# Performance work log

Measured on AMD Instinct MI355X. Metric: run time of the kernel, lower is better.

The kernel has to match this reference:

```python
import jax, jax.numpy as jnp
import numpy as np

V, DS, DF, H, NPASS = 32000, 64, 256, 8, 2
B, L, NB = 2, 1024, 512
EPS = 1e-5


def setup_inputs() -> dict:
    ks = jax.random.split(jax.random.key(0), 20)
    def n(k, shape, scale=0.02):
        return (scale * jax.random.normal(k, shape)).astype(jnp.float32)
    return {
        "token_ids": jax.random.randint(ks[0], (B, L), 0, V),
        "tok_mu": n(ks[1], (V, DS)),
        "tok_log_var": n(ks[2], (V, DS)),
        "tok_raw_alpha": n(ks[3], (V, 1), 1.0),
        "tok_features": n(ks[4], (V, DF)),
        "pos_mu": n(ks[5], (L, DS)),
        "qproj_w": n(ks[6], (H * DS, DS)),
        "qproj_b": jnp.zeros((H * DS,), jnp.float32),
        "hproj_w": n(ks[7], (DF, H * DF)),
        "hproj_b": jnp.zeros((DF,), jnp.float32),
        "mu_up_w": n(ks[8], (DS, 2 * DF)),
        "mu_up_b": jnp.zeros((DS,), jnp.float32),
        "agate_w": n(ks[9], (1, 2 * DF)),
        "agate_b": jnp.zeros((1,), jnp.float32),
        "ffn_w": n(ks[10], (DF, 2 * DF)),
        "ffn_b": jnp.zeros((DF,), jnp.float32),
        "ln_g": jnp.ones((DF,), jnp.float32),
        "ln_b": jnp.zeros((DF,), jnp.float32),
        "lm_w": n(ks[11], (V, DF)),
        "lm_b": jnp.zeros((V,), jnp.float32),
        "blob_mu": n(ks[12], (NB, DS)),
        "blob_lv": n(ks[13], (NB, DS)),
        "blob_ra": n(ks[14], (NB,), 1.0),
        "blob_f": n(ks[15], (NB, DF)),
        "bgate_w": n(ks[16], (1, 2 * DF)),
        "bgate_b": jnp.zeros((1,), jnp.float32),
    }


def _composite_weights(a):
    # front-to-back alpha compositing along last axis: w_j = a_j * prod_{k<j}(1-a_k)
    T = jnp.cumprod(1.0 - a, axis=-1)
    T_ex = jnp.concatenate([jnp.ones_like(T[..., :1]), T[..., :-1]], axis=-1)
    return a * T_ex, T[..., -1]


def _forward(token_ids, tok_mu, tok_log_var, tok_raw_alpha, tok_features, pos_mu,
             qproj_w, qproj_b, hproj_w, hproj_b, mu_up_w, mu_up_b, agate_w, agate_b,
             ffn_w, ffn_b, ln_g, ln_b, lm_w, lm_b, blob_mu, blob_lv, blob_ra, blob_f,
             bgate_w, bgate_b):
    Bc, Lc = token_ids.shape
    mu = tok_mu[token_ids] + pos_mu[:Lc][None]          # [B,L,DS]
    log_var = tok_log_var[token_ids]                     # [B,L,DS]
    alpha = jax.nn.sigmoid(tok_raw_alpha[token_ids][..., 0])  # [B,L]
    features = tok_features[token_ids]                   # [B,L,DF]

    # ---- blob query + blob render ----
    query = mu.mean(axis=1)                              # [B,DS]
    iv_b = jnp.exp(-blob_lv)                             # [NB,DS]
    d2b = (jnp.einsum('bd,nd->bn', query * query, iv_b)
           - 2.0 * jnp.einsum('bd,nd->bn', query, blob_mu * iv_b)
           + jnp.sum(blob_mu * blob_mu * iv_b, -1)[None])
    Kb = jnp.exp(-0.5 * d2b)                             # [B,NB]
    ab = jax.nn.sigmoid(blob_ra)[None] * Kb              # effective alpha
    wb, t_residual = _composite_weights(ab)
    blob_meaning = jnp.einsum('bn,nf->bf', wb, blob_f)   # [B,DF] (blob_proj = Identity)

    # ---- word meaning: multi-pass Gaussian causal render ----
    mask = jnp.tril(jnp.ones((Lc, Lc), jnp.float32))
    iv = jnp.exp(-log_var)                               # inv-variance, fixed across passes
    cur_mu, cur_alpha, cur_feat = mu, alpha, features
    meaning = None
    for p in range(NPASS):
        q = (cur_mu @ qproj_w.T + qproj_b).reshape(Bc, Lc, H, DS).transpose(0, 2, 1, 3)  # [B,H,L,DS]
        # squared Mahalanobis distance via three GEMM-style contractions (no [B,H,L,L,DS] tensor)
        d2 = (jnp.einsum('bhid,bjd->bhij', q * q, iv)
              - 2.0 * jnp.einsum('bhid,bjd->bhij', q, cur_mu * iv)
              + jnp.sum(cur_mu * cur_mu * iv, -1)[:, None, None, :])
        K = jnp.exp(-0.5 * d2)                           # [B,H,L,L]
        a = cur_alpha[:, None, None, :] * K * mask
        w, _ = _composite_weights(a)
        m = jnp.einsum('bhij,bjf->bhif', w, cur_feat)    # [B,H,L,DF]
        m_cat = m.transpose(0, 2, 1, 3).reshape(Bc, Lc, H * DF)
        meaning = m_cat @ hproj_w.T + hproj_b            # [B,L,DF] (dropout = eval/identity)
        if p < NPASS - 1:
            ctx = jnp.concatenate([cur_feat, meaning], axis=-1)  # [B,L,2DF]
            cur_mu = cur_mu + ctx @ mu_up_w.T + mu_up_b
            cur_alpha = cur_alpha * jax.nn.sigmoid(ctx @ agate_w.T + agate_b)[..., 0]
            cur_feat = cur_feat + ctx @ ffn_w.T + ffn_b

    # ---- blob gate fusion ----
    blob_exp = jnp.broadcast_to(blob_meaning[:, None, :], meaning.shape)
    gate = jax.nn.sigmoid(jnp.concatenate([blob_exp, meaning], -1) @ bgate_w.T + bgate_b)  # [B,L,1]
    t_res = t_residual[:, None, None]
    fused = (1.0 - t_res) * gate * blob_exp + t_res * meaning

    # ---- final layernorm + lm head ----
    mean = fused.mean(-1, keepdims=True)
    var = ((fused - mean) ** 2).mean(-1, keepdims=True)
    h = (fused - mean) * jax.lax.rsqrt(var + EPS) * ln_g + ln_b
    logits = h @ lm_w.T + lm_b                           # [B,L,V]
    return logits


def reference(token_ids, tok_mu, tok_log_var, tok_raw_alpha, tok_features, pos_mu,
              qproj_w, qproj_b, hproj_w, hproj_b, mu_up_w, mu_up_b, agate_w, agate_b,
              ffn_w, ffn_b, ln_g, ln_b, lm_w, lm_b, blob_mu, blob_lv, blob_ra, blob_f,
              bgate_w, bgate_b):
    return _forward(token_ids, tok_mu, tok_log_var, tok_raw_alpha, tok_features, pos_mu,
                    qproj_w, qproj_b, hproj_w, hproj_b, mu_up_w, mu_up_b, agate_w, agate_b,
                    ffn_w, ffn_b, ln_g, ln_b, lm_w, lm_b, blob_mu, blob_lv, blob_ra, blob_f,
                    bgate_w, bgate_b)
```

## Files before the change

kernel.cpp:

```cpp
#include <hip/hip_runtime.h>
#include <hip/hip_bf16.h>
#include <cstdint>
#include <cstddef>

#define V_   32000
#define DS_  64
#define DF_  256
#define H_   8
#define L_   1024
#define B_   2
#define NB_  512
#define BL_  2048
#define EPS_ 1e-5f

typedef unsigned short ushort_t;
typedef unsigned int uint_t;
typedef short bf16x8 __attribute__((ext_vector_type(8)));
typedef float f32x4 __attribute__((ext_vector_type(4)));
#define AS1 __attribute__((address_space(1)))
#define AS3 __attribute__((address_space(3)))

__device__ __forceinline__ float sigmoidf_(float x) { return 1.f / (1.f + __expf(-x)); }
__device__ __forceinline__ ushort_t f2bf(float x) {
    __hip_bfloat16 b = __float2bfloat16(x);
    return __builtin_bit_cast(ushort_t, b);
}
__device__ __forceinline__ uint_t packbf(float lo, float hi) {
    return ((uint_t)f2bf(hi) << 16) | (uint_t)f2bf(lo);
}
__device__ __forceinline__ float bflo(uint_t v) {
    return __builtin_bit_cast(float, v << 16);
}
__device__ __forceinline__ float bfhi(uint_t v) {
    return __builtin_bit_cast(float, v & 0xFFFF0000u);
}

__device__ __forceinline__ float block_reduce_sum(float v, float* red) {
    int t = threadIdx.x;
    red[t] = v;
    __syncthreads();
    for (int s = 128; s > 0; s >>= 1) {
        if (t < s) red[t] += red[t + s];
        __syncthreads();
    }
    float r = red[0];
    __syncthreads();
    return r;
}

__global__ __launch_bounds__(256) void k_cvt5(
    const float* __restrict__ s0, ushort_t* __restrict__ d0,
    const float* __restrict__ s1, ushort_t* __restrict__ d1,
    const float* __restrict__ s2, ushort_t* __restrict__ d2,
    const float* __restrict__ s3, ushort_t* __restrict__ d3,
    const float* __restrict__ s4, ushort_t* __restrict__ d4) {
    int blk = blockIdx.x;
    const float* s; ushort_t* d; int base;
    if (blk < 32)        { s = s0; d = d0; base = blk; }
    else if (blk < 64)   { s = s1; d = d1; base = blk - 32; }
    else if (blk < 192)  { s = s2; d = d2; base = blk - 64; }
    else if (blk < 704)  { s = s3; d = d3; base = blk - 192; }
    else                 { s = s4; d = d4; base = blk - 704; }
    int i = (base * 256 + threadIdx.x) * 4;
    float4 v = *reinterpret_cast<const float4*>(s + i);
    ushort4 o = {f2bf(v.x), f2bf(v.y), f2bf(v.z), f2bf(v.w)};
    *reinterpret_cast<ushort4*>(d + i) = o;
}

__global__ __launch_bounds__(256) void k_gather(
    const int* __restrict__ tok, const float* __restrict__ tok_mu,
    const float* __restrict__ tok_lv, const float* __restrict__ tok_ra,
    const float* __restrict__ tok_f, const float* __restrict__ pos_mu,
    float* __restrict__ mu, ushort_t* __restrict__ mub16,
    uint_t* __restrict__ muivP, float* __restrict__ alpha,
    float* __restrict__ feat, ushort_t* __restrict__ featb16,
    uint_t* __restrict__ featP) {
    __shared__ float sfg[256];
    int row = blockIdx.x;
    int l = row & (L_ - 1);
    int t = threadIdx.x;
    int v = tok[row];
    if (t < DS_) {
        float m = tok_mu[(size_t)v * DS_ + t] + pos_mu[l * DS_ + t];
        mu[(size_t)row * DS_ + t] = m;
        mub16[(size_t)row * DS_ + t] = f2bf(m);
        float ivv = __expf(-tok_lv[(size_t)v * DS_ + t]);
        muivP[(size_t)t * BL_ + row] = packbf(m, ivv);
    }
    float fv = tok_f[(size_t)v * DF_ + t];
    feat[(size_t)row * DF_ + t] = fv;
    featb16[(size_t)row * DF_ + t] = f2bf(fv);
    sfg[t] = fv;
    if (t == 0) alpha[row] = sigmoidf_(tok_ra[v]);
    __syncthreads();
    if (t < 128) {
        int half = t >> 6, fl = t & 63;
        featP[(size_t)row * 128 + half * 64 + fl] =
            packbf(sfg[half * 128 + fl], sfg[half * 128 + fl + 64]);
    }
}

__global__ __launch_bounds__(256) void k_queryblob(
    const float* __restrict__ mu, const float* __restrict__ blob_mu,
    const float* __restrict__ blob_lv, const float* __restrict__ blob_ra,
    const float* __restrict__ blob_f, float* __restrict__ blobm,
    float* __restrict__ tres) {
    __shared__ float red[256];
    __shared__ float sq[DS_];
    __shared__ float sa[NB_];
    __shared__ float sp[NB_];
    int b = blockIdx.x, t = threadIdx.x;
    int d = t & 63, c = t >> 6;
    float s = 0.f;
    for (int l = c; l < L_; l += 4) s += mu[((size_t)b * L_ + l) * DS_ + d];
    red[t] = s;
    __syncthreads();
    if (c == 0)
        sq[d] = (red[d] + red[64 + d] + red[128 + d] + red[192 + d]) * (1.f / L_);
    __syncthreads();
    for (int n = t; n < NB_; n += 256) {
        float d2 = 0.f;
        for (int dd = 0; dd < DS_; ++dd) {
            float diff = sq[dd] - blob_mu[n * DS_ + dd];
            d2 += __expf(-blob_lv[n * DS_ + dd]) * diff * diff;
        }
        float a = sigmoidf_(blob_ra[n]) * __expf(-0.5f * d2);
        sa[n] = a;
        sp[n] = 1.f - a;
    }
    __syncthreads();
    int n0 = t, n1 = t + 256;
    for (int s2 = 1; s2 < NB_; s2 <<= 1) {
        float t0 = (n0 >= s2) ? sp[n0 - s2] : 1.f;
        float t1 = (n1 >= s2) ? sp[n1 - s2] : 1.f;
        __syncthreads();
        sp[n0] *= t0;
        sp[n1] *= t1;
        __syncthreads();
    }
    float w0 = sa[n0] * (n0 ? sp[n0 - 1] : 1.f);
    float w1 = sa[n1] * sp[n1 - 1];
    __syncthreads();
    sa[n0] = w0;
    sa[n1] = w1;
    if (t == 0) tres[b] = sp[NB_ - 1];
    __syncthreads();
    float acc = 0.f;
    for (int n = 0; n < NB_; ++n) acc += sa[n] * blob_f[n * DF_ + t];
    blobm[b * DF_ + t] = acc;
}

__global__ __launch_bounds__(512) void k_attn3(
    const float* __restrict__ q, const uint_t* __restrict__ muivP,
    const float* __restrict__ alpha, const uint_t* __restrict__ featP,
    ushort_t* __restrict__ mcatb) {
    __shared__ uint_t smiu[64 * 64];
    __shared__ uint_t sfp[64 * 128];
    __shared__ float sq[H_][64];
    __shared__ float swt[H_][64];
    __shared__ float sT[H_];
    int tid = threadIdx.x;
    int w = tid >> 6, lane = tid & 63;
    int bid = blockIdx.x;
    int b = bid >> 10, i = bid & (L_ - 1);
    int row = b * L_ + i;

    sq[w][lane] = q[(size_t)row * 512 + tid];
    float T = 1.f;
    float a0 = 0.f, a1 = 0.f, a2 = 0.f, a3 = 0.f;

    for (int j0 = 0; j0 <= i; j0 += 64) {
        __syncthreads();
        if (j0 > 0) {
            bool alive = false;
            #pragma unroll
            for (int h = 0; h < H_; ++h) alive |= (sT[h] >= 1e-12f);
            if (!alive) break;
        }
        {
            const uint_t* src = muivP + b * L_ + j0;
            #pragma unroll
            for (int r = 0; r < 2; ++r) {
                int d = w * 8 + r * 4 + (lane >> 4);
                const uint_t* gp = src + (size_t)d * BL_ + (lane & 15) * 4;
                __builtin_amdgcn_global_load_lds((const AS1 uint_t*)gp,
                    (AS3 uint_t*)&smiu[(w * 8 + r * 4) * 64], 16, 0, 0);
            }
            const uint_t* fsrc = featP + (size_t)(b * L_ + j0) * 128 + w * 1024;
            #pragma unroll
            for (int it = 0; it < 4; ++it) {
                __builtin_amdgcn_global_load_lds((const AS1 uint_t*)(fsrc + it * 256 + lane * 4),
                    (AS3 uint_t*)&sfp[w * 1024 + it * 256], 16, 0, 0);
            }
        }
        __syncthreads();

        int jj = j0 + lane;
        float d2 = 0.f;
        #pragma unroll 8
        for (int d = 0; d < 64; ++d) {
            uint_t v = smiu[d * 64 + lane];
            float m = bflo(v), iv = bfhi(v);
            float diff = sq[w][d] - m;
            d2 = fmaf(iv * diff, diff, d2);
        }
        float a = (jj <= i) ? alpha[b * L_ + jj] * __expf(-0.5f * d2) : 0.f;

        float p = 1.f - a;
        #pragma unroll
        for (int s = 1; s < 64; s <<= 1) {
            float tt = __shfl_up(p, s, 64);
            if (lane >= s) p *= tt;
        }
        float Tex = __shfl_up(p, 1, 64);
        if (lane == 0) Tex = 1.f;
        swt[w][lane] = a * T * Tex;
        float Tch = __shfl(p, 63, 64);
        unsigned long long dead = __ballot(p < 1e-12f);
        int jn = i - j0 + 1;
        if (jn > 64) jn = 64;
        if (dead) {
            int cut = __builtin_ctzll(dead) + 1;
            if (cut < jn) jn = cut;
        }
        T *= Tch;
        if (lane == 0) sT[w] = T;

        for (int j = 0; j < jn; ++j) {
            float wj = swt[w][j];
            uint_t v0 = sfp[j * 128 + lane];
            uint_t v1 = sfp[j * 128 + 64 + lane];
            a0 = fmaf(wj, bflo(v0), a0);
            a1 = fmaf(wj, bfhi(v0), a1);
            a2 = fmaf(wj, bflo(v1), a2);
            a3 = fmaf(wj, bfhi(v1), a3);
        }
    }
    ushort_t* o = mcatb + (size_t)row * 2048 + w * 256 + lane;
    o[0] = f2bf(a0); o[64] = f2bf(a1); o[128] = f2bf(a2); o[192] = f2bf(a3);
}

template <int BM, int BN, int BK, int WGM, int WGN, bool NTS, bool WB16>
__global__ __launch_bounds__(256) void gemm_mfma2(
    const ushort_t* __restrict__ A, const ushort_t* __restrict__ A2, int K1,
    int strideA, const ushort_t* __restrict__ W, const float* __restrict__ bias,
    float* __restrict__ C, ushort_t* __restrict__ Cb, int M, int N, int K) {
    constexpr int WMF = BM / WGM / 16;
    constexpr int WNF = BN / WGN / 16;
    constexpr int KK  = BK / 32;
    constexpr int AHALF = BM * BK;
    constexpr int BHALF = BN * BK;
    constexpr int STAGE_B = 2 * (AHALF + BHALF) * 2;
    constexpr int EPI_B = BM * BN * 4;
    constexpr int SMEM_B = STAGE_B > EPI_B ? STAGE_B : EPI_B;
    __shared__ __align__(16) char smem[SMEM_B];
    ushort_t* As = (ushort_t*)smem;
    ushort_t* Bs = (ushort_t*)(smem + 2 * AHALF * 2);

    const int tid = threadIdx.x;
    const int wave = tid >> 6, lane = tid & 63;
    const int m0 = blockIdx.x * BM, n0 = blockIdx.y * BN;
    const int wr = wave / WGN, wc = wave % WGN;
    const int lr = lane & 15;
    const int q4 = lane >> 4;

    f32x4 acc[WMF][WNF] = {};

    auto stage = [&](int buf, int t) {
        const int k0g = t * BK;
        const ushort_t* Abase = (A2 != nullptr && k0g >= K1) ? A2 : A;
        const int kof = (A2 != nullptr && k0g >= K1) ? k0g - K1 : k0g;
        ushort_t* Ad = As + buf * AHALF;
        #pragma unroll
        for (int it = 0; it < (BM * BK / 8) / 256; ++it) {
            int cbase = it * 256 + wave * 64;
            int c = cbase + lane;
            int r = c & (BM - 1), c8 = c / BM;
            const ushort_t* gp = Abase + (size_t)(m0 + r) * strideA + kof + c8 * 8;
            __builtin_amdgcn_global_load_lds((const AS1 uint_t*)gp,
                                             (AS3 uint_t*)(Ad + cbase * 8), 16, 0, 0);
        }
        ushort_t* Bd = Bs + buf * BHALF;
        #pragma unroll
        for (int it = 0; it < (BN * BK / 8) / 256; ++it) {
            int cbase = it * 256 + wave * 64;
            int c = cbase + lane;
            int r = c & (BN - 1), c8 = c / BN;
            const ushort_t* gp = W + (size_t)(n0 + r) * K + k0g + c8 * 8;
            __builtin_amdgcn_global_load_lds((const AS1 uint_t*)gp,
                                             (AS3 uint_t*)(Bd + cbase * 8), 16, 0, 0);
        }
    };

    const int nsteps = K / BK;
    stage(0, 0);
    __syncthreads();
    for (int t = 0; t < nsteps; ++t) {
        const int cur = t & 1;
        if (t + 1 < nsteps) stage(cur ^ 1, t + 1);
        const ushort_t* Ab = As + cur * AHALF;
        const ushort_t* Bb = Bs + cur * BHALF;
        bf16x8 af[WMF][KK], bfr[WNF][KK];
        #pragma unroll
        for (int mi = 0; mi < WMF; ++mi)
            #pragma unroll
            for (int kk = 0; kk < KK; ++kk)
                af[mi][kk] = *reinterpret_cast<const bf16x8*>(
                    &Ab[((kk * 4 + q4) * BM + wr * (BM / WGM) + mi * 16 + lr) * 8]);
        #pragma unroll
        for (int ni = 0; ni < WNF; ++ni)
            #pragma unroll
            for (int kk = 0; kk < KK; ++kk)
                bfr[ni][kk] = *reinterpret_cast<const bf16x8*>(
                    &Bb[((kk * 4 + q4) * BN + wc * (BN / WGN) + ni * 16 + lr) * 8]);
        #pragma unroll
        for (int kk = 0; kk < KK; ++kk)
            #pragma unroll
            for (int mi = 0; mi < WMF; ++mi)
                #pragma unroll
                for (int ni = 0; ni < WNF; ++ni)
                    acc[mi][ni] = __builtin_amdgcn_mfma_f32_16x16x32_bf16(
                        af[mi][kk], bfr[ni][kk], acc[mi][ni], 0, 0, 0);
        __syncthreads();
    }

    float* tile = (float*)smem;
    #pragma unroll
    for (int mi = 0; mi < WMF; ++mi)
        #pragma unroll
        for (int ni = 0; ni < WNF; ++ni) {
            int col = wc * (BN / WGN) + ni * 16 + lr;
            float bv = bias[n0 + col];
            #pragma unroll
            for (int j = 0; j < 4; ++j) {
                int r2 = wr * (BM / WGM) + mi * 16 + q4 * 4 + j;
                tile[r2 * BN + col] = acc[mi][ni][j] + bv;
            }
        }
    __syncthreads();
    constexpr int EV = (BM * BN / 4) / 256;
    #pragma unroll
    for (int e = 0; e < EV; ++e) {
        int idx = e * 256 + tid;
        int r = idx / (BN / 4), c4 = idx % (BN / 4);
        f32x4 v = reinterpret_cast<const f32x4*>(tile)[idx];
        f32x4* dst = reinterpret_cast<f32x4*>(&C[(size_t)(m0 + r) * N + n0 + c4 * 4]);
        if (NTS) __builtin_nontemporal_store(v, dst);
        else *dst = v;
        if (WB16) {
            ushort4 ob = {f2bf(v[0]), f2bf(v[1]), f2bf(v[2]), f2bf(v[3])};
            *reinterpret_cast<ushort4*>(&Cb[(size_t)(m0 + r) * N + n0 + c4 * 4]) = ob;
        }
    }
}

__global__ __launch_bounds__(256) void k_apply(
    const float* __restrict__ meaning, const float* __restrict__ agw,
    const float* __restrict__ agb, const float* __restrict__ dmu,
    const float* __restrict__ dffn, float* __restrict__ mu,
    ushort_t* __restrict__ mub16, uint_t* __restrict__ muivP,
    float* __restrict__ alpha, float* __restrict__ feat,
    ushort_t* __restrict__ featb16, uint_t* __restrict__ featP) {
    __shared__ float red[256];
    int row = blockIdx.x, t = threadIdx.x;
    float c0 = feat[(size_t)row * DF_ + t];
    float c1 = meaning[(size_t)row * DF_ + t];
    float s = block_reduce_sum(c0 * agw[t] + c1 * agw[256 + t], red);
    if (t == 0) alpha[row] *= sigmoidf_(s + agb[0]);
    if (t < DS_) {
        float m = mu[(size_t)row * DS_ + t] + dmu[(size_t)row * DS_ + t];
        mu[(size_t)row * DS_ + t] = m;
        mub16[(size_t)row * DS_ + t] = f2bf(m);
        uint_t v = muivP[(size_t)t * BL_ + row];
        muivP[(size_t)t * BL_ + row] = (v & 0xFFFF0000u) | (uint_t)f2bf(m);
    }
    float fn = c0 + dffn[(size_t)row * DF_ + t];
    feat[(size_t)row * DF_ + t] = fn;
    featb16[(size_t)row * DF_ + t] = f2bf(fn);
    red[t] = fn;
    __syncthreads();
    if (t < 128) {
        int half = t >> 6, fl = t & 63;
        featP[(size_t)row * 128 + half * 64 + fl] =
            packbf(red[half * 128 + fl], red[half * 128 + fl + 64]);
    }
}

__global__ __launch_bounds__(256) void k_fused_ln(
    const float* __restrict__ meaning, const float* __restrict__ blobm,
    const float* __restrict__ tres, const float* __restrict__ bgw,
    const float* __restrict__ bgb, const float* __restrict__ ln_g,
    const float* __restrict__ ln_b, ushort_t* __restrict__ houtb) {
    __shared__ float red[256];
    int row = blockIdx.x, t = threadIdx.x;
    int b = row >> 10;
    float m = meaning[(size_t)row * DF_ + t];
    float be = blobm[b * DF_ + t];
    float tr = tres[b];
    float gsum = block_reduce_sum(be * bgw[t] + m * bgw[256 + t], red);
    float gate = sigmoidf_(gsum + bgb[0]);
    float f = (1.f - tr) * gate * be + tr * m;
    float mean = block_reduce_sum(f, red) * (1.f / DF_);
    float d = f - mean;
    float var = block_reduce_sum(d * d, red) * (1.f / DF_);
    houtb[(size_t)row * DF_ + t] = f2bf(d * rsqrtf(var + EPS_) * ln_g[t] + ln_b[t]);
}

extern "C" void kernel_launch(void* const* d_in, const int* in_sizes, int n_in,
                              void* d_out, int out_size, void* d_ws, size_t ws_size,
                              hipStream_t stream) {
    const int*   tok      = (const int*)d_in[0];
    const float* tok_mu   = (const float*)d_in[1];
    const float* tok_lv   = (const float*)d_in[2];
    const float* tok_ra   = (const float*)d_in[3];
    const float* tok_f    = (const float*)d_in[4];
    const float* pos_mu   = (const float*)d_in[5];
    const float* qproj_w  = (const float*)d_in[6];
    const float* qproj_b  = (const float*)d_in[7];
    const float* hproj_w  = (const float*)d_in[8];
    const float* hproj_b  = (const float*)d_in[9];
    const float* mu_up_w  = (const float*)d_in[10];
    const float* mu_up_b  = (const float*)d_in[11];
    const float* agate_w  = (const float*)d_in[12];
    const float* agate_b  = (const float*)d_in[13];
    const float* ffn_w    = (const float*)d_in[14];
    const float* ffn_b    = (const float*)d_in[15];
    const float* ln_g     = (const float*)d_in[16];
    const float* ln_b     = (const float*)d_in[17];
    const float* lm_w     = (const float*)d_in[18];
    const float* lm_b     = (const float*)d_in[19];
    const float* blob_mu  = (const float*)d_in[20];
    const float* blob_lv  = (const float*)d_in[21];
    const float* blob_ra  = (const float*)d_in[22];
    const float* blob_f   = (const float*)d_in[23];
    const float* bgate_w  = (const float*)d_in[24];
    const float* bgate_b  = (const float*)d_in[25];
    float* out = (float*)d_out;

    float* ws = (float*)d_ws;
    float* mu      = ws;
    float* alpha   = mu + BL_ * DS_;
    float* feat    = alpha + BL_;
    float* blobm   = feat + BL_ * DF_;
    float* tres    = blobm + B_ * DF_;
    float* q       = tres + 64;
    float* meaning = q + BL_ * 512;
    float* dmu     = meaning + BL_ * DF_;
    float* dffn    = dmu + BL_ * DS_;
    uint_t* muivP  = (uint_t*)(dffn + BL_ * DF_);
    uint_t* featP  = muivP + (size_t)DS_ * BL_;
    ushort_t* mub16 = (ushort_t*)(featP + (size_t)BL_ * 128);
    ushort_t* featb16 = mub16 + (size_t)BL_ * DS_;
    ushort_t* meanb16 = featb16 + (size_t)BL_ * DF_;
    ushort_t* mcatb = meanb16 + (size_t)BL_ * DF_;
    ushort_t* hbufb = mcatb + (size_t)BL_ * 2048;
    ushort_t* wbf   = hbufb + (size_t)BL_ * DF_;
    ushort_t* hpwbf = wbf + (size_t)V_ * DF_;
    ushort_t* qpwbf = hpwbf + (size_t)DF_ * 2048;
    ushort_t* muwbf = qpwbf + (size_t)512 * 64;
    ushort_t* ffnwbf = muwbf + (size_t)64 * 512;

    k_cvt5<<<8704, 256, 0, stream>>>(qproj_w, qpwbf, mu_up_w, muwbf,
                                     ffn_w, ffnwbf, hproj_w, hpwbf, lm_w, wbf);

    k_gather<<<BL_, 256, 0, stream>>>(tok, tok_mu, tok_lv, tok_ra, tok_f, pos_mu,
                                      mu, mub16, muivP, alpha, feat, featb16, featP);
    k_queryblob<<<B_, 256, 0, stream>>>(mu, blob_mu, blob_lv, blob_ra, blob_f,
                                        blobm, tres);

    for (int p = 0; p < 2; ++p) {
        gemm_mfma2<32, 32, 64, 2, 2, false, false>
            <<<dim3(BL_ / 32, 512 / 32), 256, 0, stream>>>(
            mub16, nullptr, 0, DS_, qpwbf, qproj_b, q, nullptr, BL_, 512, DS_);
        k_attn3<<<BL_, 512, 0, stream>>>(q, muivP, alpha, featP, mcatb);
        if (p == 0) {
            gemm_mfma2<32, 32, 64, 2, 2, false, true>
                <<<dim3(BL_ / 32, DF_ / 32), 256, 0, stream>>>(
                mcatb, nullptr, 0, H_ * DF_, hpwbf, hproj_b, meaning, meanb16,
                BL_, DF_, H_ * DF_);
            gemm_mfma2<32, 32, 64, 2, 2, false, false>
                <<<dim3(BL_ / 32, DS_ / 32), 256, 0, stream>>>(
                featb16, meanb16, DF_, DF_, muwbf, mu_up_b, dmu, nullptr,
                BL_, DS_, 512);
            gemm_mfma2<32, 32, 64, 2, 2, false, false>
                <<<dim3(BL_ / 32, DF_ / 32), 256, 0, stream>>>(
                featb16, meanb16, DF_, DF_, ffnwbf, ffn_b, dffn, nullptr,
                BL_, DF_, 512);
            k_apply<<<BL_, 256, 0, stream>>>(meaning, agate_w, agate_b, dmu, dffn,
                                             mu, mub16, muivP, alpha, feat,
                                             featb16, featP);
        } else {
            gemm_mfma2<32, 32, 64, 2, 2, false, false>
                <<<dim3(BL_ / 32, DF_ / 32), 256, 0, stream>>>(
                mcatb, nullptr, 0, H_ * DF_, hpwbf, hproj_b, meaning, nullptr,
                BL_, DF_, H_ * DF_);
        }
    }

    k_fused_ln<<<BL_, 256, 0, stream>>>(meaning, blobm, tres, bgate_w, bgate_b,
                                        ln_g, ln_b, hbufb);
    gemm_mfma2<128, 128, 64, 2, 2, true, false>
        <<<dim3(BL_ / 128, V_ / 128), 256, 0, stream>>>(
        hbufb, nullptr, 0, DF_, wbf, lm_b, out, nullptr, BL_, V_, DF_);
}
```

Before: 332.4 us.

## Fuse setup kernels, compute query projection inside attention, merge mu/ffn GEMMs

Merges the weight conversion, token gather and blob-query kernels into one k_setup launch. The query-projection GEMM is dropped and q is computed in fp32 inside the attention kernel from mu and qproj_w. The mu_up and ffn GEMMs become a single 320-wide GEMM with concatenated weights and bias. The packed mu/ivar and feature layouts change to 8-byte pairs for wider LDS reads. This cuts launch count and intermediate traffic, at the cost of redundant per-block q computation and a mixed-role setup kernel where 256 of 512 threads sit idle in most blocks.

After: 376.9 us. 13.4% more time.

```diff
diff --git a/kernel.cpp b/kernel.cpp
--- a/kernel.cpp
+++ b/kernel.cpp
@@ -17,6 +17,7 @@
 typedef unsigned int uint_t;
 typedef short bf16x8 __attribute__((ext_vector_type(8)));
 typedef float f32x4 __attribute__((ext_vector_type(4)));
+typedef unsigned int uint2x __attribute__((ext_vector_type(2)));
 #define AS1 __attribute__((address_space(1)))
 #define AS3 __attribute__((address_space(3)))
 
@@ -48,114 +49,128 @@
     return r;
 }
 
-__global__ __launch_bounds__(256) void k_cvt5(
-    const float* __restrict__ s0, ushort_t* __restrict__ d0,
-    const float* __restrict__ s1, ushort_t* __restrict__ d1,
-    const float* __restrict__ s2, ushort_t* __restrict__ d2,
-    const float* __restrict__ s3, ushort_t* __restrict__ d3,
-    const float* __restrict__ s4, ushort_t* __restrict__ d4) {
-    int blk = blockIdx.x;
-    const float* s; ushort_t* d; int base;
-    if (blk < 32)        { s = s0; d = d0; base = blk; }
-    else if (blk < 64)   { s = s1; d = d1; base = blk - 32; }
-    else if (blk < 192)  { s = s2; d = d2; base = blk - 64; }
-    else if (blk < 704)  { s = s3; d = d3; base = blk - 192; }
-    else                 { s = s4; d = d4; base = blk - 704; }
-    int i = (base * 256 + threadIdx.x) * 4;
-    float4 v = *reinterpret_cast<const float4*>(s + i);
-    ushort4 o = {f2bf(v.x), f2bf(v.y), f2bf(v.z), f2bf(v.w)};
-    *reinterpret_cast<ushort4*>(d + i) = o;
-}
-
-__global__ __launch_bounds__(256) void k_gather(
+#define NCVT_   8672
+#define NGATH_  (NCVT_ + BL_)
+#define NQB_    (NGATH_ + B_)
+__global__ __launch_bounds__(512) void k_setup(
     const int* __restrict__ tok, const float* __restrict__ tok_mu,
     const float* __restrict__ tok_lv, const float* __restrict__ tok_ra,
     const float* __restrict__ tok_f, const float* __restrict__ pos_mu,
-    float* __restrict__ mu, ushort_t* __restrict__ mub16,
-    uint_t* __restrict__ muivP, float* __restrict__ alpha,
-    float* __restrict__ feat, ushort_t* __restrict__ featb16,
-    uint_t* __restrict__ featP) {
-    __shared__ float sfg[256];
-    int row = blockIdx.x;
-    int l = row & (L_ - 1);
-    int t = threadIdx.x;
-    int v = tok[row];
-    if (t < DS_) {
-        float m = tok_mu[(size_t)v * DS_ + t] + pos_mu[l * DS_ + t];
-        mu[(size_t)row * DS_ + t] = m;
-        mub16[(size_t)row * DS_ + t] = f2bf(m);
-        float ivv = __expf(-tok_lv[(size_t)v * DS_ + t]);
-        muivP[(size_t)t * BL_ + row] = packbf(m, ivv);
-    }
-    float fv = tok_f[(size_t)v * DF_ + t];
-    feat[(size_t)row * DF_ + t] = fv;
-    featb16[(size_t)row * DF_ + t] = f2bf(fv);
-    sfg[t] = fv;
-    if (t == 0) alpha[row] = sigmoidf_(tok_ra[v]);
-    __syncthreads();
-    if (t < 128) {
-        int half = t >> 6, fl = t & 63;
-        featP[(size_t)row * 128 + half * 64 + fl] =
-            packbf(sfg[half * 128 + fl], sfg[half * 128 + fl + 64]);
-    }
-}
-
-__global__ __launch_bounds__(256) void k_queryblob(
-    const float* __restrict__ mu, const float* __restrict__ blob_mu,
-    const float* __restrict__ blob_lv, const float* __restrict__ blob_ra,
-    const float* __restrict__ blob_f, float* __restrict__ blobm,
-    float* __restrict__ tres) {
-    __shared__ float red[256];
-    __shared__ float sq[DS_];
-    __shared__ float sa[NB_];
-    __shared__ float sp[NB_];
-    int b = blockIdx.x, t = threadIdx.x;
-    int d = t & 63, c = t >> 6;
-    float s = 0.f;
-    for (int l = c; l < L_; l += 4) s += mu[((size_t)b * L_ + l) * DS_ + d];
-    red[t] = s;
-    __syncthreads();
-    if (c == 0)
-        sq[d] = (red[d] + red[64 + d] + red[128 + d] + red[192 + d]) * (1.f / L_);
-    __syncthreads();
-    for (int n = t; n < NB_; n += 256) {
-        float d2 = 0.f;
-        for (int dd = 0; dd < DS_; ++dd) {
-            float diff = sq[dd] - blob_mu[n * DS_ + dd];
-            d2 += __expf(-blob_lv[n * DS_ + dd]) * diff * diff;
-        }
-        float a = sigmoidf_(blob_ra[n]) * __expf(-0.5f * d2);
-        sa[n] = a;
-        sp[n] = 1.f - a;
-    }
-    __syncthreads();
-    int n0 = t, n1 = t + 256;
-    for (int s2 = 1; s2 < NB_; s2 <<= 1) {
-        float t0 = (n0 >= s2) ? sp[n0 - s2] : 1.f;
-        float t1 = (n1 >= s2) ? sp[n1 - s2] : 1.f;
-        __syncthreads();
-        sp[n0] *= t0;
-        sp[n1] *= t1;
-        __syncthreads();
-    }
-    float w0 = sa[n0] * (n0 ? sp[n0 - 1] : 1.f);
-    float w1 = sa[n1] * sp[n1 - 1];
-    __syncthreads();
-    sa[n0] = w0;
-    sa[n1] = w1;
-    if (t == 0) tres[b] = sp[NB_ - 1];
-    __syncthreads();
-    float acc = 0.f;
-    for (int n = 0; n < NB_; ++n) acc += sa[n] * blob_f[n * DF_ + t];
-    blobm[b * DF_ + t] = acc;
-}
-
-__global__ __launch_bounds__(512) void k_attn3(
-    const float* __restrict__ q, const uint_t* __restrict__ muivP,
-    const float* __restrict__ alpha, const uint_t* __restrict__ featP,
+    const float* __restrict__ mu_up_w, const float* __restrict__ ffn_w,
+    const float* __restrict__ hproj_w, const float* __restrict__ lm_w,
+    const float* __restrict__ mu_up_b, const float* __restrict__ ffn_b,
+    const float* __restrict__ blob_mu, const float* __restrict__ blob_lv,
+    const float* __restrict__ blob_ra, const float* __restrict__ blob_f,
+    ushort_t* __restrict__ cwbf, ushort_t* __restrict__ hpwbf,
+    ushort_t* __restrict__ wbf, float* __restrict__ cbias,
+    float* __restrict__ mu, uint_t* __restrict__ muivP2,
+    float* __restrict__ alpha, float* __restrict__ feat,
+    ushort_t* __restrict__ featb16, uint2x* __restrict__ fArr,
+    float* __restrict__ blobm, float* __restrict__ tres) {
+    int blk = blockIdx.x;
+    int tid = threadIdx.x;
+    if (blk < NCVT_) {
+        if (tid >= 256) return;
+        const float* s; ushort_t* d; int base;
+        if (blk < 32)        { s = mu_up_w; d = cwbf;          base = blk; }
+        else if (blk < 160)  { s = ffn_w;   d = cwbf + 32768;  base = blk - 32; }
+        else if (blk < 672)  { s = hproj_w; d = hpwbf;         base = blk - 160; }
+        else                 { s = lm_w;    d = wbf;           base = blk - 672; }
+        int i = (base * 256 + tid) * 4;
+        float4 v = *reinterpret_cast<const float4*>(s + i);
+        ushort4 o = {f2bf(v.x), f2bf(v.y), f2bf(v.z), f2bf(v.w)};
+        *reinterpret_cast<ushort4*>(d + i) = o;
+        return;
+    }
+    if (blk < NGATH_) {
+        if (tid >= 256) return;
+        __shared__ float sfg[256];
+        int row = blk - NCVT_;
+        int l = row & (L_ - 1);
+        int v = tok[row];
+        if (tid < DS_) {
+            float m = tok_mu[(size_t)v * DS_ + tid] + pos_mu[l * DS_ + tid];
+            mu[(size_t)row * DS_ + tid] = m;
+            float ivv = __expf(-tok_lv[(size_t)v * DS_ + tid]);
+            muivP2[((size_t)(tid >> 1) * BL_ + row) * 2 + (tid & 1)] = packbf(m, ivv);
+        }
+        float fv = tok_f[(size_t)v * DF_ + tid];
+        feat[(size_t)row * DF_ + tid] = fv;
+        featb16[(size_t)row * DF_ + tid] = f2bf(fv);
+        sfg[tid] = fv;
+        if (tid == 0) alpha[row] = sigmoidf_(tok_ra[v]);
+        __syncthreads();
+        if (tid < 64) {
+            uint2x pp;
+            pp.x = packbf(sfg[tid], sfg[tid + 64]);
+            pp.y = packbf(sfg[tid + 128], sfg[tid + 192]);
+            fArr[(size_t)row * 64 + tid] = pp;
+        }
+        return;
+    }
+    if (blk < NQB_) {
+        if (tid >= 256) return;
+        __shared__ float red[256];
+        __shared__ int stok[L_];
+        __shared__ float sq[DS_];
+        __shared__ float sa[NB_];
+        __shared__ float sp[NB_];
+        int b = blk - NGATH_;
+        for (int l = tid; l < L_; l += 256) stok[l] = tok[b * L_ + l];
+        __syncthreads();
+        int d = tid & 63, c = tid >> 6;
+        float s = 0.f;
+        for (int l = c; l < L_; l += 4)
+            s += tok_mu[(size_t)stok[l] * DS_ + d] + pos_mu[l * DS_ + d];
+        red[tid] = s;
+        __syncthreads();
+        if (c == 0)
+            sq[d] = (red[d] + red[64 + d] + red[128 + d] + red[192 + d]) * (1.f / L_);
+        __syncthreads();
+        for (int n = tid; n < NB_; n += 256) {
+            float d2 = 0.f;
+            for (int dd = 0; dd < DS_; ++dd) {
+                float diff = sq[dd] - blob_mu[n * DS_ + dd];
+                d2 += __expf(-blob_lv[n * DS_ + dd]) * diff * diff;
+            }
+            float a = sigmoidf_(blob_ra[n]) * __expf(-0.5f * d2);
+            sa[n] = a;
+            sp[n] = 1.f - a;
+        }
+        __syncthreads();
+        int n0 = tid, n1 = tid + 256;
+        for (int s2 = 1; s2 < NB_; s2 <<= 1) {
+            float t0 = (n0 >= s2) ? sp[n0 - s2] : 1.f;
+            float t1 = (n1 >= s2) ? sp[n1 - s2] : 1.f;
+            __syncthreads();
+            sp[n0] *= t0;
+            sp[n1] *= t1;
+            __syncthreads();
+        }
+        float w0 = sa[n0] * (n0 ? sp[n0 - 1] : 1.f);
+        float w1 = sa[n1] * sp[n1 - 1];
+        __syncthreads();
+        sa[n0] = w0;
+        sa[n1] = w1;
+        if (tid == 0) tres[b] = sp[NB_ - 1];
+        __syncthreads();
+        float acc = 0.f;
+        for (int n = 0; n < NB_; ++n) acc += sa[n] * blob_f[n * DF_ + tid];
+        blobm[b * DF_ + tid] = acc;
+        return;
+    }
+    if (tid < 64) cbias[tid] = mu_up_b[tid];
+    if (tid < 256) cbias[64 + tid] = ffn_b[tid];
+}
+
+__global__ __launch_bounds__(512) void k_attn4(
+    const float* __restrict__ mu, const float* __restrict__ qw,
+    const float* __restrict__ qb, const uint2x* __restrict__ muivP2,
+    const float* __restrict__ alpha, const uint2x* __restrict__ fArr,
     ushort_t* __restrict__ mcatb) {
-    __shared__ uint_t smiu[64 * 64];
-    __shared__ uint_t sfp[64 * 128];
+    __shared__ uint2x smiu[32 * 64];
+    __shared__ uint2x sfp[64 * 64];
+    __shared__ float smu[DS_];
     __shared__ float sq[H_][64];
     __shared__ float swt[H_][64];
     __shared__ float sT[H_];
@@ -165,7 +180,20 @@
     int b = bid >> 10, i = bid & (L_ - 1);
     int row = b * L_ + i;
 
-    sq[w][lane] = q[(size_t)row * 512 + tid];
+    if (tid < DS_) smu[tid] = mu[(size_t)row * DS_ + tid];
+    __syncthreads();
+    {
+        float qv = qb[tid];
+        const float4* qwr = reinterpret_cast<const float4*>(qw + (size_t)tid * DS_);
+        #pragma unroll
+        for (int k = 0; k < 16; ++k) {
+            float4 v = qwr[k];
+            qv += v.x * smu[k * 4] + v.y * smu[k * 4 + 1] +
+                  v.z * smu[k * 4 + 2] + v.w * smu[k * 4 + 3];
+        }
+        sq[w][lane] = qv;
+    }
+
     float T = 1.f;
     float a0 = 0.f, a1 = 0.f, a2 = 0.f, a3 = 0.f;
 
@@ -177,34 +205,37 @@
             for (int h = 0; h < H_; ++h) alive |= (sT[h] >= 1e-12f);
             if (!alive) break;
         }
-        {
-            const uint_t* src = muivP + b * L_ + j0;
-            #pragma unroll
-            for (int r = 0; r < 2; ++r) {
-                int d = w * 8 + r * 4 + (lane >> 4);
-                const uint_t* gp = src + (size_t)d * BL_ + (lane & 15) * 4;
-                __builtin_amdgcn_global_load_lds((const AS1 uint_t*)gp,
-                    (AS3 uint_t*)&smiu[(w * 8 + r * 4) * 64], 16, 0, 0);
-            }
-            const uint_t* fsrc = featP + (size_t)(b * L_ + j0) * 128 + w * 1024;
-            #pragma unroll
-            for (int it = 0; it < 4; ++it) {
-                __builtin_amdgcn_global_load_lds((const AS1 uint_t*)(fsrc + it * 256 + lane * 4),
-                    (AS3 uint_t*)&sfp[w * 1024 + it * 256], 16, 0, 0);
-            }
+        #pragma unroll
+        for (int r = 0; r < 2; ++r) {
+            int d2r = w * 4 + r * 2;
+            const uint2x* gp = muivP2 + (size_t)(d2r + (lane >> 5)) * BL_ +
+                               (b * L_ + j0) + (lane & 31) * 2;
+            __builtin_amdgcn_global_load_lds((const AS1 uint_t*)gp,
+                (AS3 uint_t*)&smiu[d2r * 64], 16, 0, 0);
+        }
+        #pragma unroll
+        for (int it = 0; it < 4; ++it) {
+            int jr = w * 8 + it * 2;
+            const uint2x* gp = fArr + (size_t)(b * L_ + j0 + jr + (lane >> 5)) * 64 +
+                               (lane & 31) * 2;
+            __builtin_amdgcn_global_load_lds((const AS1 uint_t*)gp,
+                (AS3 uint_t*)&sfp[jr * 64], 16, 0, 0);
         }
         __syncthreads();
 
         int jj = j0 + lane;
-        float d2 = 0.f;
+        float d2a = 0.f;
         #pragma unroll 8
-        for (int d = 0; d < 64; ++d) {
-            uint_t v = smiu[d * 64 + lane];
-            float m = bflo(v), iv = bfhi(v);
-            float diff = sq[w][d] - m;
-            d2 = fmaf(iv * diff, diff, d2);
-        }
-        float a = (jj <= i) ? alpha[b * L_ + jj] * __expf(-0.5f * d2) : 0.f;
+        for (int d2 = 0; d2 < 32; ++d2) {
+            uint2x v = smiu[d2 * 64 + lane];
+            float m0 = bflo(v.x), iv0 = bfhi(v.x);
+            float m1 = bflo(v.y), iv1 = bfhi(v.y);
+            float f0 = sq[w][2 * d2] - m0;
+            float f1 = sq[w][2 * d2 + 1] - m1;
+            d2a = fmaf(iv0 * f0, f0, d2a);
+            d2a = fmaf(iv1 * f1, f1, d2a);
+        }
+        float a = (jj <= i) ? alpha[b * L_ + jj] * __expf(-0.5f * d2a) : 0.f;
 
         float p = 1.f - a;
         #pragma unroll
@@ -228,12 +259,11 @@
 
         for (int j = 0; j < jn; ++j) {
             float wj = swt[w][j];
-            uint_t v0 = sfp[j * 128 + lane];
-            uint_t v1 = sfp[j * 128 + 64 + lane];
-            a0 = fmaf(wj, bflo(v0), a0);
-            a1 = fmaf(wj, bfhi(v0), a1);
-            a2 = fmaf(wj, bflo(v1), a2);
-            a3 = fmaf(wj, bfhi(v1), a3);
+            uint2x v = sfp[j * 64 + lane];
+            a0 = fmaf(wj, bflo(v.x), a0);
+            a1 = fmaf(wj, bfhi(v.x), a1);
+            a2 = fmaf(wj, bflo(v.y), a2);
+            a3 = fmaf(wj, bfhi(v.y), a3);
         }
     }
     ushort_t* o = mcatb + (size_t)row * 2048 + w * 256 + lane;
@@ -356,11 +386,10 @@
 
 __global__ __launch_bounds__(256) void k_apply(
     const float* __restrict__ meaning, const float* __restrict__ agw,
-    const float* __restrict__ agb, const float* __restrict__ dmu,
-    const float* __restrict__ dffn, float* __restrict__ mu,
-    ushort_t* __restrict__ mub16, uint_t* __restrict__ muivP,
+    const float* __restrict__ agb, const float* __restrict__ dctx,
+    float* __restrict__ mu, uint_t* __restrict__ muivP2,
     float* __restrict__ alpha, float* __restrict__ feat,
-    ushort_t* __restrict__ featb16, uint_t* __restrict__ featP) {
+    ushort_t* __restrict__ featb16, uint2x* __restrict__ fArr) {
     __shared__ float red[256];
     int row = blockIdx.x, t = threadIdx.x;
     float c0 = feat[(size_t)row * DF_ + t];
@@ -368,21 +397,22 @@
     float s = block_reduce_sum(c0 * agw[t] + c1 * agw[256 + t], red);
     if (t == 0) alpha[row] *= sigmoidf_(s + agb[0]);
     if (t < DS_) {
-        float m = mu[(size_t)row * DS_ + t] + dmu[(size_t)row * DS_ + t];
+        float m = mu[(size_t)row * DS_ + t] + dctx[(size_t)row * 320 + t];
         mu[(size_t)row * DS_ + t] = m;
-        mub16[(size_t)row * DS_ + t] = f2bf(m);
-        uint_t v = muivP[(size_t)t * BL_ + row];
-        muivP[(size_t)t * BL_ + row] = (v & 0xFFFF0000u) | (uint_t)f2bf(m);
-    }
-    float fn = c0 + dffn[(size_t)row * DF_ + t];
+        size_t idx = ((size_t)(t >> 1) * BL_ + row) * 2 + (t & 1);
+        uint_t v = muivP2[idx];
+        muivP2[idx] = (v & 0xFFFF0000u) | (uint_t)f2bf(m);
+    }
+    float fn = c0 + dctx[(size_t)row * 320 + 64 + t];
     feat[(size_t)row * DF_ + t] = fn;
     featb16[(size_t)row * DF_ + t] = f2bf(fn);
     red[t] = fn;
     __syncthreads();
-    if (t < 128) {
-        int half = t >> 6, fl = t & 63;
-        featP[(size_t)row * 128 + half * 64 + fl] =
-            packbf(red[half * 128 + fl], red[half * 128 + fl + 64]);
+    if (t < 64) {
+        uint2x pp;
+        pp.x = packbf(red[t], red[t + 64]);
+        pp.y = packbf(red[t + 128], red[t + 192]);
+        fArr[(size_t)row * 64 + t] = pp;
     }
 }
 
@@ -443,52 +473,41 @@
     float* feat    = alpha + BL_;
     float* blobm   = feat + BL_ * DF_;
     float* tres    = blobm + B_ * DF_;
-    float* q       = tres + 64;
-    float* meaning = q + BL_ * 512;
-    float* dmu     = meaning + BL_ * DF_;
-    float* dffn    = dmu + BL_ * DS_;
-    uint_t* muivP  = (uint_t*)(dffn + BL_ * DF_);
-    uint_t* featP  = muivP + (size_t)DS_ * BL_;
-    ushort_t* mub16 = (ushort_t*)(featP + (size_t)BL_ * 128);
-    ushort_t* featb16 = mub16 + (size_t)BL_ * DS_;
+    float* meaning = tres + 64;
+    float* dctx    = meaning + BL_ * DF_;
+    float* cbias   = dctx + (size_t)BL_ * 320;
+    uint_t* muivP2u = (uint_t*)(cbias + 384);
+    uint2x* muivP2  = (uint2x*)muivP2u;
+    uint2x* fArr    = (uint2x*)(muivP2u + 131072);
+    ushort_t* featb16 = (ushort_t*)(fArr + (size_t)BL_ * 64);
     ushort_t* meanb16 = featb16 + (size_t)BL_ * DF_;
     ushort_t* mcatb = meanb16 + (size_t)BL_ * DF_;
     ushort_t* hbufb = mcatb + (size_t)BL_ * 2048;
     ushort_t* wbf   = hbufb + (size_t)BL_ * DF_;
     ushort_t* hpwbf = wbf + (size_t)V_ * DF_;
-    ushort_t* qpwbf = hpwbf + (size_t)DF_ * 2048;
-    ushort_t* muwbf = qpwbf + (size_t)512 * 64;
-    ushort_t* ffnwbf = muwbf + (size_t)64 * 512;
-
-    k_cvt5<<<8704, 256, 0, stream>>>(qproj_w, qpwbf, mu_up_w, muwbf,
-                                     ffn_w, ffnwbf, hproj_w, hpwbf, lm_w, wbf);
-
-    k_gather<<<BL_, 256, 0, stream>>>(tok, tok_mu, tok_lv, tok_ra, tok_f, pos_mu,
-                                      mu, mub16, muivP, alpha, feat, featb16, featP);
-    k_queryblob<<<B_, 256, 0, stream>>>(mu, blob_mu, blob_lv, blob_ra, blob_f,
-                                        blobm, tres);
+    ushort_t* cwbf  = hpwbf + (size_t)DF_ * 2048;
+
+    k_setup<<<NQB_ + 1, 512, 0, stream>>>(
+        tok, tok_mu, tok_lv, tok_ra, tok_f, pos_mu, mu_up_w, ffn_w, hproj_w,
+        lm_w, mu_up_b, ffn_b, blob_mu, blob_lv, blob_ra, blob_f,
+        cwbf, hpwbf, wbf, cbias, mu, muivP2u, alpha, feat, featb16, fArr,
+        blobm, tres);
 
     for (int p = 0; p < 2; ++p) {
-        gemm_mfma2<32, 32, 64, 2, 2, false, false>
-            <<<dim3(BL_ / 32, 512 / 32), 256, 0, stream>>>(
-            mub16, nullptr, 0, DS_, qpwbf, qproj_b, q, nullptr, BL_, 512, DS_);
-        k_attn3<<<BL_, 512, 0, stream>>>(q, muivP, alpha, featP, mcatb);
+        k_attn4<<<BL_, 512, 0, stream>>>(mu, qproj_w, qproj_b, muivP2, alpha,
+                                         fArr, mcatb);
         if (p == 0) {
             gemm_mfma2<32, 32, 64, 2, 2, false, true>
                 <<<dim3(BL_ / 32, DF_ / 32), 256, 0, stream>>>(
                 mcatb, nullptr, 0, H_ * DF_, hpwbf, hproj_b, meaning, meanb16,
                 BL_, DF_, H_ * DF_);
             gemm_mfma2<32, 32, 64, 2, 2, false, false>
-                <<<dim3(BL_ / 32, DS_ / 32), 256, 0, stream>>>(
-                featb16, meanb16, DF_, DF_, muwbf, mu_up_b, dmu, nullptr,
-                BL_, DS_, 512);
-            gemm_mfma2<32, 32, 64, 2, 2, false, false>
-                <<<dim3(BL_ / 32, DF_ / 32), 256, 0, stream>>>(
-                featb16, meanb16, DF_, DF_, ffnwbf, ffn_b, dffn, nullptr,
-                BL_, DF_, 512);
-            k_apply<<<BL_, 256, 0, stream>>>(meaning, agate_w, agate_b, dmu, dffn,
-                                             mu, mub16, muivP, alpha, feat,
-                                             featb16, featP);
+                <<<dim3(BL_ / 32, 320 / 32), 256, 0, stream>>>(
+                featb16, meanb16, DF_, DF_, cwbf, cbias, dctx, nullptr,
+                BL_, 320, 512);
+            k_apply<<<BL_, 256, 0, stream>>>(meaning, agate_w, agate_b, dctx,
+                                             mu, muivP2u, alpha, feat,
+                                             featb16, fArr);
         } else {
             gemm_mfma2<32, 32, 64, 2, 2, false, false>
                 <<<dim3(BL_ / 32, DF_ / 32), 256, 0, stream>>>(
```

## Use MFMA for attention feature accumulation with transposed swizzled feature layout

Applied to the files above, without the earlier changes.

The per-wave scalar loop that accumulates weighted features over keys is replaced by bf16 16x16x32 MFMA instructions. Composite weights for all 8 heads are stored as bf16 in shared memory, and features are kept in a transposed, XOR-swizzled global layout so they can be loaded straight into LDS for B fragments. The early-exit trimming of the per-chunk key count (dead transmittance cutoff) is removed, so every chunk processes all 64 keys. Weights are rounded to bf16, which adds error, and an extra block sync per chunk is introduced.

New measurement: 314.9 us. 1.06x faster.

```diff
diff --git a/kernel.cpp b/kernel.cpp
--- a/kernel.cpp
+++ b/kernel.cpp
@@ -74,9 +74,9 @@
     float* __restrict__ mu, ushort_t* __restrict__ mub16,
     uint_t* __restrict__ muivP, float* __restrict__ alpha,
     float* __restrict__ feat, ushort_t* __restrict__ featb16,
-    uint_t* __restrict__ featP) {
-    __shared__ float sfg[256];
+    ushort_t* __restrict__ fTg) {
     int row = blockIdx.x;
+    int b = row >> 10;
     int l = row & (L_ - 1);
     int t = threadIdx.x;
     int v = tok[row];
@@ -90,14 +90,12 @@
     float fv = tok_f[(size_t)v * DF_ + t];
     feat[(size_t)row * DF_ + t] = fv;
     featb16[(size_t)row * DF_ + t] = f2bf(fv);
-    sfg[t] = fv;
+    {
+        int jb = (l >> 3) & 7, jr = l & 7;
+        int jp = (l & ~63) | ((jb ^ (t & 7)) << 3) | jr;
+        fTg[((size_t)(b * DF_ + t) << 10) + jp] = f2bf(fv);
+    }
     if (t == 0) alpha[row] = sigmoidf_(tok_ra[v]);
-    __syncthreads();
-    if (t < 128) {
-        int half = t >> 6, fl = t & 63;
-        featP[(size_t)row * 128 + half * 64 + fl] =
-            packbf(sfg[half * 128 + fl], sfg[half * 128 + fl + 64]);
-    }
 }
 
 __global__ __launch_bounds__(256) void k_queryblob(
@@ -150,24 +148,27 @@
     blobm[b * DF_ + t] = acc;
 }
 
-__global__ __launch_bounds__(512) void k_attn3(
+__global__ __launch_bounds__(512) void k_attn5(
     const float* __restrict__ q, const uint_t* __restrict__ muivP,
-    const float* __restrict__ alpha, const uint_t* __restrict__ featP,
+    const float* __restrict__ alpha, const ushort_t* __restrict__ fTg,
     ushort_t* __restrict__ mcatb) {
-    __shared__ uint_t smiu[64 * 64];
-    __shared__ uint_t sfp[64 * 128];
+    __shared__ __align__(16) uint_t smiu[64 * 64];
+    __shared__ __align__(16) ushort_t sfT[256 * 64];
+    __shared__ __align__(16) ushort_t sw16[16][72];
     __shared__ float sq[H_][64];
-    __shared__ float swt[H_][64];
     __shared__ float sT[H_];
     int tid = threadIdx.x;
     int w = tid >> 6, lane = tid & 63;
     int bid = blockIdx.x;
     int b = bid >> 10, i = bid & (L_ - 1);
     int row = b * L_ + i;
-
+    const int lr = lane & 15, q4 = lane >> 4;
+
+    for (int k = tid; k < 16 * 72; k += 512) ((ushort_t*)sw16)[k] = 0;
     sq[w][lane] = q[(size_t)row * 512 + tid];
+
     float T = 1.f;
-    float a0 = 0.f, a1 = 0.f, a2 = 0.f, a3 = 0.f;
+    f32x4 acc0 = {}, acc1 = {};
 
     for (int j0 = 0; j0 <= i; j0 += 64) {
         __syncthreads();
@@ -181,30 +182,34 @@
             const uint_t* src = muivP + b * L_ + j0;
             #pragma unroll
             for (int r = 0; r < 2; ++r) {
-                int d = w * 8 + r * 4 + (lane >> 4);
-                const uint_t* gp = src + (size_t)d * BL_ + (lane & 15) * 4;
+                int d = w * 8 + r * 4 + q4;
+                const uint_t* gp = src + (size_t)d * BL_ + lr * 4;
                 __builtin_amdgcn_global_load_lds((const AS1 uint_t*)gp,
                     (AS3 uint_t*)&smiu[(w * 8 + r * 4) * 64], 16, 0, 0);
             }
-            const uint_t* fsrc = featP + (size_t)(b * L_ + j0) * 128 + w * 1024;
+        }
+        {
             #pragma unroll
             for (int it = 0; it < 4; ++it) {
-                __builtin_amdgcn_global_load_lds((const AS1 uint_t*)(fsrc + it * 256 + lane * 4),
-                    (AS3 uint_t*)&sfp[w * 1024 + it * 256], 16, 0, 0);
+                int c0 = w * 32 + it * 8;
+                const ushort_t* gp = fTg +
+                    ((size_t)(b * DF_ + c0 + (lane >> 3)) << 10) + j0 + (lane & 7) * 8;
+                __builtin_amdgcn_global_load_lds((const AS1 uint_t*)gp,
+                    (AS3 uint_t*)&sfT[c0 * 64], 16, 0, 0);
             }
         }
         __syncthreads();
 
         int jj = j0 + lane;
-        float d2 = 0.f;
+        float d2a = 0.f;
         #pragma unroll 8
         for (int d = 0; d < 64; ++d) {
             uint_t v = smiu[d * 64 + lane];
             float m = bflo(v), iv = bfhi(v);
             float diff = sq[w][d] - m;
-            d2 = fmaf(iv * diff, diff, d2);
-        }
-        float a = (jj <= i) ? alpha[b * L_ + jj] * __expf(-0.5f * d2) : 0.f;
+            d2a = fmaf(iv * diff, diff, d2a);
+        }
+        float a = (jj <= i) ? alpha[b * L_ + jj] * __expf(-0.5f * d2a) : 0.f;
 
         float p = 1.f - a;
         #pragma unroll
@@ -214,30 +219,40 @@
         }
         float Tex = __shfl_up(p, 1, 64);
         if (lane == 0) Tex = 1.f;
-        swt[w][lane] = a * T * Tex;
+        sw16[w][lane] = f2bf(a * T * Tex);
         float Tch = __shfl(p, 63, 64);
-        unsigned long long dead = __ballot(p < 1e-12f);
-        int jn = i - j0 + 1;
-        if (jn > 64) jn = 64;
-        if (dead) {
-            int cut = __builtin_ctzll(dead) + 1;
-            if (cut < jn) jn = cut;
-        }
         T *= Tch;
         if (lane == 0) sT[w] = T;
-
-        for (int j = 0; j < jn; ++j) {
-            float wj = swt[w][j];
-            uint_t v0 = sfp[j * 128 + lane];
-            uint_t v1 = sfp[j * 128 + 64 + lane];
-            a0 = fmaf(wj, bflo(v0), a0);
-            a1 = fmaf(wj, bfhi(v0), a1);
-            a2 = fmaf(wj, bflo(v1), a2);
-            a3 = fmaf(wj, bfhi(v1), a3);
-        }
-    }
-    ushort_t* o = mcatb + (size_t)row * 2048 + w * 256 + lane;
-    o[0] = f2bf(a0); o[64] = f2bf(a1); o[128] = f2bf(a2); o[192] = f2bf(a3);
+        __syncthreads();
+
+        #pragma unroll
+        for (int kk = 0; kk < 2; ++kk) {
+            bf16x8 afr = *reinterpret_cast<const bf16x8*>(
+                (const char*)sw16 + lr * 144 + kk * 64 + q4 * 16);
+            {
+                int c = (w * 2 + 0) * 16 + lr;
+                int bo = c * 128 + ((kk * 64 + q4 * 16) ^ ((c & 7) << 4));
+                bf16x8 bfr = *reinterpret_cast<const bf16x8*>((const char*)sfT + bo);
+                acc0 = __builtin_amdgcn_mfma_f32_16x16x32_bf16(afr, bfr, acc0, 0, 0, 0);
+            }
+            {
+                int c = (w * 2 + 1) * 16 + lr;
+                int bo = c * 128 + ((kk * 64 + q4 * 16) ^ ((c & 7) << 4));
+                bf16x8 bfr = *reinterpret_cast<const bf16x8*>((const char*)sfT + bo);
+                acc1 = __builtin_amdgcn_mfma_f32_16x16x32_bf16(afr, bfr, acc1, 0, 0, 0);
+            }
+        }
+    }
+    if (q4 < 2) {
+        #pragma unroll
+        for (int r = 0; r < 4; ++r) {
+            int h = q4 * 4 + r;
+            int c0 = (w * 2 + 0) * 16 + lr;
+            int c1 = (w * 2 + 1) * 16 + lr;
+            mcatb[(size_t)row * 2048 + h * 256 + c0] = f2bf(acc0[r]);
+            mcatb[(size_t)row * 2048 + h * 256 + c1] = f2bf(acc1[r]);
+        }
+    }
 }
 
 template <int BM, int BN, int BK, int WGM, int WGN, bool NTS, bool WB16>
@@ -360,9 +375,11 @@
     const float* __restrict__ dffn, float* __restrict__ mu,
     ushort_t* __restrict__ mub16, uint_t* __restrict__ muivP,
     float* __restrict__ alpha, float* __restrict__ feat,
-    ushort_t* __restrict__ featb16, uint_t* __restrict__ featP) {
+    ushort_t* __restrict__ featb16, ushort_t* __restrict__ fTg) {
     __shared__ float red[256];
     int row = blockIdx.x, t = threadIdx.x;
+    int b = row >> 10;
+    int l = row & (L_ - 1);
     float c0 = feat[(size_t)row * DF_ + t];
     float c1 = meaning[(size_t)row * DF_ + t];
     float s = block_reduce_sum(c0 * agw[t] + c1 * agw[256 + t], red);
@@ -377,12 +394,10 @@
     float fn = c0 + dffn[(size_t)row * DF_ + t];
     feat[(size_t)row * DF_ + t] = fn;
     featb16[(size_t)row * DF_ + t] = f2bf(fn);
-    red[t] = fn;
-    __syncthreads();
-    if (t < 128) {
-        int half = t >> 6, fl = t & 63;
-        featP[(size_t)row * 128 + half * 64 + fl] =
-            packbf(red[half * 128 + fl], red[half * 128 + fl + 64]);
+    {
+        int jb = (l >> 3) & 7, jr = l & 7;
+        int jp = (l & ~63) | ((jb ^ (t & 7)) << 3) | jr;
+        fTg[((size_t)(b * DF_ + t) << 10) + jp] = f2bf(fn);
     }
 }
 
@@ -448,8 +463,8 @@
     float* dmu     = meaning + BL_ * DF_;
     float* dffn    = dmu + BL_ * DS_;
     uint_t* muivP  = (uint_t*)(dffn + BL_ * DF_);
-    uint_t* featP  = muivP + (size_t)DS_ * BL_;
-    ushort_t* mub16 = (ushort_t*)(featP + (size_t)BL_ * 128);
+    ushort_t* fTg   = (ushort_t*)(muivP + (size_t)DS_ * BL_);
+    ushort_t* mub16 = fTg + (size_t)B_ * DF_ * L_;
     ushort_t* featb16 = mub16 + (size_t)BL_ * DS_;
     ushort_t* meanb16 = featb16 + (size_t)BL_ * DF_;
     ushort_t* mcatb = meanb16 + (size_t)BL_ * DF_;
@@ -464,7 +479,7 @@
                                      ffn_w, ffnwbf, hproj_w, hpwbf, lm_w, wbf);
 
     k_gather<<<BL_, 256, 0, stream>>>(tok, tok_mu, tok_lv, tok_ra, tok_f, pos_mu,
-                                      mu, mub16, muivP, alpha, feat, featb16, featP);
+                                      mu, mub16, muivP, alpha, feat, featb16, fTg);
     k_queryblob<<<B_, 256, 0, stream>>>(mu, blob_mu, blob_lv, blob_ra, blob_f,
                                         blobm, tres);
 
@@ -472,7 +487,7 @@
         gemm_mfma2<32, 32, 64, 2, 2, false, false>
             <<<dim3(BL_ / 32, 512 / 32), 256, 0, stream>>>(
             mub16, nullptr, 0, DS_, qpwbf, qproj_b, q, nullptr, BL_, 512, DS_);
-        k_attn3<<<BL_, 512, 0, stream>>>(q, muivP, alpha, featP, mcatb);
+        k_attn5<<<BL_, 512, 0, stream>>>(q, muivP, alpha, fTg, mcatb);
         if (p == 0) {
             gemm_mfma2<32, 32, 64, 2, 2, false, true>
                 <<<dim3(BL_ / 32, DF_ / 32), 256, 0, stream>>>(
@@ -488,7 +503,7 @@
                 BL_, DF_, 512);
             k_apply<<<BL_, 256, 0, stream>>>(meaning, agate_w, agate_b, dmu, dffn,
                                              mu, mub16, muivP, alpha, feat,
-                                             featb16, featP);
+                                             featb16, fTg);
         } else {
             gemm_mfma2<32, 32, 64, 2, 2, false, false>
                 <<<dim3(BL_ / 32, DF_ / 32), 256, 0, stream>>>(
```
